# Optimization experiments

Measured on AMD Instinct MI355X. Metric: run time of the kernel, lower is better.

The kernel has to match this reference:

```python
import jax, jax.numpy as jnp
import numpy as np

MASK_VALUE = -1000000.0  # matches torch source's value=-1000000.0


def setup_inputs() -> dict:
    key = jax.random.key(0)
    kq, kk, kv, kl = jax.random.split(key, 4)
    B, S, D = 64, 1024, 64
    q = jax.random.normal(kq, (B, S, D), dtype=jnp.float32)
    k = jax.random.normal(kk, (B, S, D), dtype=jnp.float32)
    v = jax.random.normal(kv, (B, S, D), dtype=jnp.float32)
    valid_lens = jax.random.randint(kl, (B,), 0, S, dtype=jnp.int32)
    return {"q": q, "k": k, "v": v, "valid_lens": valid_lens}


def reference(q, k, v, valid_lens):
    # scores: [B, Sq, Sk]
    d = q.shape[-1]
    scores = jnp.einsum("bqd,bkd->bqk", q, k) / jnp.sqrt(jnp.float32(d))
    # 1-D valid_lens broadcast over the query dim (torch repeat_interleave branch)
    Sk = k.shape[1]
    mask = jnp.arange(Sk, dtype=jnp.int32)[None, None, :] < valid_lens[:, None, None]
    scores = jnp.where(mask, scores, MASK_VALUE)
    attn = jax.nn.softmax(scores, axis=-1)
    # dropout p=0.0 -> identity (eval-mode reference)
    return jnp.einsum("bqk,bkd->bqd", attn, v)
```

## Files before the change

kernel.cpp:

```cpp
#include <hip/hip_runtime.h>
#include <math.h>


#define BATCH 64
#define SEQ   1024
#define DIM   64
#define BQ    64
#define BC    64
#define NKT   (SEQ / BC)
#define HALFT 8
#define LSTR  72
#define QSCALE 0.18033688011112442f
#define MASKED -1.0e6f

#define WS_LM_SZ   (2048 * 64 * 8)
#define WS_O_OFF   WS_LM_SZ
#define WS_O_SZ    (2048 * 4096 * 4)
#define WS_NEEDED  ((size_t)WS_O_OFF + (size_t)WS_O_SZ)

typedef __attribute__((ext_vector_type(8))) short bf16x8;
typedef __attribute__((ext_vector_type(4))) float f32x4;

__device__ __forceinline__ uint pack2_trunc(float lo, float hi) {
    return __builtin_amdgcn_perm(__float_as_uint(hi), __float_as_uint(lo), 0x07060302);
}
__device__ __forceinline__ ushort f2bf_rne(float x) {
    uint u = __float_as_uint(x);
    return (ushort)((u + 0x7fffu + ((u >> 16) & 1u)) >> 16);
}

__global__ __launch_bounds__(256, 4) void attn_mfma_splitk(
    const float* __restrict__ q, const float* __restrict__ k,
    const float* __restrict__ v, const int* __restrict__ valid_lens,
    float* __restrict__ out,
    float2* __restrict__ lmbuf, float* __restrict__ opart)
{
    __shared__ ushort KPs[BC * LSTR];
    __shared__ ushort Vt[DIM * LSTR];

    const int t    = threadIdx.x;
    const int wave = t >> 6;
    const int wl   = t & 63;
    const int QD   = wl >> 4;
    const int li   = wl & 15;
    const int g    = blockIdx.x;
    const int grp  = g >> 6;
    const int b    = ((g & 63) + grp) & 63;
    const int half = grp & 1;
    const int qt   = grp >> 1;
    const int q0   = qt * BQ;
    const int pid  = (qt << 6) | b;
    const int item = pid * 2 + half;
    const int vl   = valid_lens[b];

    const size_t boff = (size_t)b * SEQ * DIM;

    const int it_full  = (vl == 0) ? NKT : ((vl + BC - 1) >> 6);
    const int it_begin = half * HALFT;
    const int it_end   = min(it_full, it_begin + HALFT);

    if (it_begin >= it_end) return;

    const bool direct = (half == 0) && (it_full <= HALFT);

    bf16x8 qb[2];
    {
        const float* qrow = q + boff + (size_t)(q0 + wave * 16 + li) * DIM + QD * 8;
        #pragma unroll
        for (int kc = 0; kc < 2; kc++) {
            float4 a = *(const float4*)(qrow + kc * 32);
            float4 c = *(const float4*)(qrow + kc * 32 + 4);
            union { bf16x8 v; ushort u[8]; } tmp;
            tmp.u[0] = f2bf_rne(a.x * QSCALE);
            tmp.u[1] = f2bf_rne(a.y * QSCALE);
            tmp.u[2] = f2bf_rne(a.z * QSCALE);
            tmp.u[3] = f2bf_rne(a.w * QSCALE);
            tmp.u[4] = f2bf_rne(c.x * QSCALE);
            tmp.u[5] = f2bf_rne(c.y * QSCALE);
            tmp.u[6] = f2bf_rne(c.z * QSCALE);
            tmp.u[7] = f2bf_rne(c.w * QSCALE);
            qb[kc] = tmp.v;
        }
    }

    float4 kf[4];
    float  vf[2][8];

    auto load_tile = [&](int it) {
        const float4* kg = (const float4*)(k + boff + (size_t)it * BC * DIM);
        #pragma unroll
        for (int i = 0; i < 4; i++) kf[i] = kg[t + 256 * i];
        const float* vgf = v + boff + (size_t)it * BC * DIM;
        #pragma unroll
        for (int i = 0; i < 2; i++) {
            int slot = t + 256 * i;
            int d = slot & 63, ko = slot >> 6;
            #pragma unroll
            for (int j = 0; j < 8; j++)
                vf[i][j] = vgf[(size_t)(ko * 8 + j) * DIM + d];
        }
    };

    auto stage = [&]() {
        #pragma unroll
        for (int i = 0; i < 4; i++) {
            int idx = t + 256 * i;
            int row = idx >> 4, c4 = idx & 15;
            uint2 w;
            w.x = pack2_trunc(kf[i].x, kf[i].y);
            w.y = pack2_trunc(kf[i].z, kf[i].w);
            *(uint2*)&KPs[row * LSTR + c4 * 4] = w;
        }
        #pragma unroll
        for (int i = 0; i < 2; i++) {
            int slot = t + 256 * i;
            int d = slot & 63, ko = slot >> 6;
            uint4 w;
            w.x = pack2_trunc(vf[i][0], vf[i][1]);
            w.y = pack2_trunc(vf[i][2], vf[i][3]);
            w.z = pack2_trunc(vf[i][4], vf[i][5]);
            w.w = pack2_trunc(vf[i][6], vf[i][7]);
            *(uint4*)&Vt[d * LSTR + ko * 8] = w;
        }
    };

    float m_run = -INFINITY, l_run = 0.f;
    f32x4 acc[4];
    #pragma unroll
    for (int dt = 0; dt < 4; dt++) acc[dt] = (f32x4){0.f, 0.f, 0.f, 0.f};

    load_tile(it_begin);

    for (int it = it_begin; it < it_end; it++) {
        __syncthreads();
        stage();
        if (it + 1 < it_end) load_tile(it + 1);
        __syncthreads();

        f32x4 sc[4];
        #pragma unroll
        for (int kt = 0; kt < 4; kt++) {
            bf16x8 ka0 = *(const bf16x8*)&KPs[(kt * 16 + li) * LSTR + QD * 8];
            bf16x8 ka1 = *(const bf16x8*)&KPs[(kt * 16 + li) * LSTR + 32 + QD * 8];
            f32x4 c = (f32x4){0.f, 0.f, 0.f, 0.f};
            c = __builtin_amdgcn_mfma_f32_16x16x32_bf16(ka0, qb[0], c, 0, 0, 0);
            c = __builtin_amdgcn_mfma_f32_16x16x32_bf16(ka1, qb[1], c, 0, 0, 0);
            sc[kt] = c;
        }

        __syncthreads();

        const int kbase = it * BC;
        if (kbase + BC > vl) {
            #pragma unroll
            for (int kt = 0; kt < 4; kt++)
                #pragma unroll
                for (int r = 0; r < 4; r++) {
                    int key = kbase + kt * 16 + QD * 4 + r;
                    if (key >= vl) sc[kt][r] = MASKED;
                }
        }

        float mt = -INFINITY;
        #pragma unroll
        for (int kt = 0; kt < 4; kt++)
            #pragma unroll
            for (int r = 0; r < 4; r++) mt = fmaxf(mt, sc[kt][r]);
        mt = fmaxf(mt, __shfl_xor(mt, 16, 64));
        mt = fmaxf(mt, __shfl_xor(mt, 32, 64));
        float mn = fmaxf(m_run, mt);
        float alpha = exp2f(m_run - mn);
        m_run = mn;

        float ls = 0.f;
        #pragma unroll
        for (int kt = 0; kt < 4; kt++) {
            float p0 = exp2f(sc[kt][0] - mn);
            float p1 = exp2f(sc[kt][1] - mn);
            float p2 = exp2f(sc[kt][2] - mn);
            float p3 = exp2f(sc[kt][3] - mn);
            ls += (p0 + p1) + (p2 + p3);
            uint2 w;
            w.x = pack2_trunc(p0, p1);
            w.y = pack2_trunc(p2, p3);
            *(uint2*)&KPs[(wave * 16 + li) * LSTR + kt * 16 + QD * 4] = w;
        }
        ls += __shfl_xor(ls, 16, 64);
        ls += __shfl_xor(ls, 32, 64);
        l_run = l_run * alpha + ls;

        float a0 = __shfl(alpha, QD * 4 + 0, 64);
        float a1 = __shfl(alpha, QD * 4 + 1, 64);
        float a2 = __shfl(alpha, QD * 4 + 2, 64);
        float a3 = __shfl(alpha, QD * 4 + 3, 64);
        #pragma unroll
        for (int dt = 0; dt < 4; dt++) {
            acc[dt][0] *= a0; acc[dt][1] *= a1;
            acc[dt][2] *= a2; acc[dt][3] *= a3;
        }

        bf16x8 pa0 = *(const bf16x8*)&KPs[(wave * 16 + li) * LSTR + QD * 8];
        bf16x8 pa1 = *(const bf16x8*)&KPs[(wave * 16 + li) * LSTR + 32 + QD * 8];
        #pragma unroll
        for (int dt = 0; dt < 4; dt++) {
            bf16x8 vb0 = *(const bf16x8*)&Vt[(dt * 16 + li) * LSTR + QD * 8];
            bf16x8 vb1 = *(const bf16x8*)&Vt[(dt * 16 + li) * LSTR + 32 + QD * 8];
            acc[dt] = __builtin_amdgcn_mfma_f32_16x16x32_bf16(pa0, vb0, acc[dt], 0, 0, 0);
            acc[dt] = __builtin_amdgcn_mfma_f32_16x16x32_bf16(pa1, vb1, acc[dt], 0, 0, 0);
        }
    }

    if (direct) {
        float invl = 1.0f / l_run;
        float i0 = __shfl(invl, QD * 4 + 0, 64);
        float i1 = __shfl(invl, QD * 4 + 1, 64);
        float i2 = __shfl(invl, QD * 4 + 2, 64);
        float i3 = __shfl(invl, QD * 4 + 3, 64);
        float* ob = out + boff + (size_t)q0 * DIM;
        const int rbase = wave * 16 + QD * 4;
        #pragma unroll
        for (int dt = 0; dt < 4; dt++) {
            int col = dt * 16 + li;
            ob[(size_t)(rbase + 0) * DIM + col] = acc[dt][0] * i0;
            ob[(size_t)(rbase + 1) * DIM + col] = acc[dt][1] * i1;
            ob[(size_t)(rbase + 2) * DIM + col] = acc[dt][2] * i2;
            ob[(size_t)(rbase + 3) * DIM + col] = acc[dt][3] * i3;
        }
    } else {
        if (QD == 0)
            lmbuf[(size_t)item * 64 + wave * 16 + li] = make_float2(m_run, l_run);
        float* ob = opart + (size_t)item * (BQ * DIM);
        const int rbase = wave * 16 + QD * 4;
        #pragma unroll
        for (int dt = 0; dt < 4; dt++) {
            int col = dt * 16 + li;
            ob[(size_t)(rbase + 0) * DIM + col] = acc[dt][0];
            ob[(size_t)(rbase + 1) * DIM + col] = acc[dt][1];
            ob[(size_t)(rbase + 2) * DIM + col] = acc[dt][2];
            ob[(size_t)(rbase + 3) * DIM + col] = acc[dt][3];
        }
    }
}

__global__ __launch_bounds__(256) void attn_combine(
    const int* __restrict__ valid_lens,
    const float2* __restrict__ lmbuf, const float* __restrict__ opart,
    float* __restrict__ out)
{
    const int pid = blockIdx.x;
    const int b   = pid & 63;
    const int qt  = pid >> 6;
    const int vl  = valid_lens[b];
    const int it_full = (vl == 0) ? NKT : ((vl + BC - 1) >> 6);
    if (it_full <= HALFT) return;

    const int t  = threadIdx.x;
    const int qr = t >> 2;
    const int c4 = t & 3;
    const int i1 = pid * 2;

    float2 ml1 = lmbuf[(size_t)i1 * 64 + qr];
    float2 ml2 = lmbuf[(size_t)(i1 + 1) * 64 + qr];
    float M  = fmaxf(ml1.x, ml2.x);
    float w1 = exp2f(ml1.x - M);
    float w2 = exp2f(ml2.x - M);
    float inv = 1.f / (ml1.y * w1 + ml2.y * w2);
    w1 *= inv; w2 *= inv;

    const float4* o1 = (const float4*)(opart + (size_t)i1 * (BQ * DIM));
    const float4* o2 = (const float4*)(opart + (size_t)(i1 + 1) * (BQ * DIM));
    float4* ob = (float4*)(out + ((size_t)b * SEQ + (size_t)qt * BQ) * DIM);
    #pragma unroll
    for (int j = 0; j < 4; j++) {
        int idx = qr * 16 + j * 4 + c4;
        float4 a  = o1[idx];
        float4 bb = o2[idx];
        float4 r;
        r.x = a.x * w1 + bb.x * w2;
        r.y = a.y * w1 + bb.y * w2;
        r.z = a.z * w1 + bb.z * w2;
        r.w = a.w * w1 + bb.w * w2;
        ob[idx] = r;
    }
}

__global__ __launch_bounds__(256, 4) void attn_mfma_flash2(
    const float* __restrict__ q, const float* __restrict__ k,
    const float* __restrict__ v, const int* __restrict__ valid_lens,
    float* __restrict__ out)
{
    __shared__ ushort Ks[BC * LSTR];
    __shared__ ushort Vt[DIM * LSTR];
    __shared__ ushort Ps[BQ * LSTR];

    const int t    = threadIdx.x;
    const int wave = t >> 6;
    const int wl   = t & 63;
    const int QD   = wl >> 4;
    const int li   = wl & 15;
    const int g    = blockIdx.x;
    const int grp  = g >> 6;
    const int b    = ((g & 63) + grp) & 63;
    const int q0   = grp * BQ;
    const int vl   = valid_lens[b];

    const size_t boff = (size_t)b * SEQ * DIM;

    bf16x8 qb[2];
    {
        const float* qrow = q + boff + (size_t)(q0 + wave * 16 + li) * DIM + QD * 8;
        #pragma unroll
        for (int kc = 0; kc < 2; kc++) {
            float4 a = *(const float4*)(qrow + kc * 32);
            float4 c = *(const float4*)(qrow + kc * 32 + 4);
            union { bf16x8 v; ushort u[8]; } tmp;
            tmp.u[0] = f2bf_rne(a.x * QSCALE);
            tmp.u[1] = f2bf_rne(a.y * QSCALE);
            tmp.u[2] = f2bf_rne(a.z * QSCALE);
            tmp.u[3] = f2bf_rne(a.w * QSCALE);
            tmp.u[4] = f2bf_rne(c.x * QSCALE);
            tmp.u[5] = f2bf_rne(c.y * QSCALE);
            tmp.u[6] = f2bf_rne(c.z * QSCALE);
            tmp.u[7] = f2bf_rne(c.w * QSCALE);
            qb[kc] = tmp.v;
        }
    }

    const int it_max = (vl == 0) ? NKT : ((vl + BC - 1) >> 6);

    float4 kf[4];
    float  vf[2][8];

    auto load_tile = [&](int it) {
        const float4* kg = (const float4*)(k + boff + (size_t)it * BC * DIM);
        #pragma unroll
        for (int i = 0; i < 4; i++) kf[i] = kg[t + 256 * i];
        const float* vgf = v + boff + (size_t)it * BC * DIM;
        #pragma unroll
        for (int i = 0; i < 2; i++) {
            int slot = t + 256 * i;
            int d = slot & 63, ko = slot >> 6;
            #pragma unroll
            for (int j = 0; j < 8; j++)
                vf[i][j] = vgf[(size_t)(ko * 8 + j) * DIM + d];
        }
    };

    auto stage = [&]() {
        #pragma unroll
        for (int i = 0; i < 4; i++) {
            int idx = t + 256 * i;
            int row = idx >> 4, c4 = idx & 15;
            uint2 w;
            w.x = pack2_trunc(kf[i].x, kf[i].y);
            w.y = pack2_trunc(kf[i].z, kf[i].w);
            *(uint2*)&Ks[row * LSTR + c4 * 4] = w;
        }
        #pragma unroll
        for (int i = 0; i < 2; i++) {
            int slot = t + 256 * i;
            int d = slot & 63, ko = slot >> 6;
            uint4 w;
            w.x = pack2_trunc(vf[i][0], vf[i][1]);
            w.y = pack2_trunc(vf[i][2], vf[i][3]);
            w.z = pack2_trunc(vf[i][4], vf[i][5]);
            w.w = pack2_trunc(vf[i][6], vf[i][7]);
            *(uint4*)&Vt[d * LSTR + ko * 8] = w;
        }
    };

    float m_run = -INFINITY, l_run = 0.f;
    f32x4 acc[4];
    #pragma unroll
    for (int dt = 0; dt < 4; dt++) acc[dt] = (f32x4){0.f, 0.f, 0.f, 0.f};

    load_tile(0);

    for (int it = 0; it < it_max; it++) {
        __syncthreads();
        stage();
        if (it + 1 < it_max) load_tile(it + 1);
        __syncthreads();

        f32x4 sc[4];
        #pragma unroll
        for (int kt = 0; kt < 4; kt++) {
            bf16x8 ka0 = *(const bf16x8*)&Ks[(kt * 16 + li) * LSTR + QD * 8];
            bf16x8 ka1 = *(const bf16x8*)&Ks[(kt * 16 + li) * LSTR + 32 + QD * 8];
            f32x4 c = (f32x4){0.f, 0.f, 0.f, 0.f};
            c = __builtin_amdgcn_mfma_f32_16x16x32_bf16(ka0, qb[0], c, 0, 0, 0);
            c = __builtin_amdgcn_mfma_f32_16x16x32_bf16(ka1, qb[1], c, 0, 0, 0);
            sc[kt] = c;
        }

        const int kbase = it * BC;
        if (kbase + BC > vl) {
            #pragma unroll
            for (int kt = 0; kt < 4; kt++)
                #pragma unroll
                for (int r = 0; r < 4; r++) {
                    int key = kbase + kt * 16 + QD * 4 + r;
                    if (key >= vl) sc[kt][r] = MASKED;
                }
        }

        float mt = -INFINITY;
        #pragma unroll
        for (int kt = 0; kt < 4; kt++)
            #pragma unroll
            for (int r = 0; r < 4; r++) mt = fmaxf(mt, sc[kt][r]);
        mt = fmaxf(mt, __shfl_xor(mt, 16, 64));
        mt = fmaxf(mt, __shfl_xor(mt, 32, 64));
        float mn = fmaxf(m_run, mt);
        float alpha = exp2f(m_run - mn);
        m_run = mn;

        float ls = 0.f;
        #pragma unroll
        for (int kt = 0; kt < 4; kt++) {
            float p0 = exp2f(sc[kt][0] - mn);
            float p1 = exp2f(sc[kt][1] - mn);
            float p2 = exp2f(sc[kt][2] - mn);
            float p3 = exp2f(sc[kt][3] - mn);
            ls += (p0 + p1) + (p2 + p3);
            uint2 w;
            w.x = pack2_trunc(p0, p1);
            w.y = pack2_trunc(p2, p3);
            *(uint2*)&Ps[(wave * 16 + li) * LSTR + kt * 16 + QD * 4] = w;
        }
        ls += __shfl_xor(ls, 16, 64);
        ls += __shfl_xor(ls, 32, 64);
        l_run = l_run * alpha + ls;

        float a0 = __shfl(alpha, QD * 4 + 0, 64);
        float a1 = __shfl(alpha, QD * 4 + 1, 64);
        float a2 = __shfl(alpha, QD * 4 + 2, 64);
        float a3 = __shfl(alpha, QD * 4 + 3, 64);
        #pragma unroll
        for (int dt = 0; dt < 4; dt++) {
            acc[dt][0] *= a0; acc[dt][1] *= a1;
            acc[dt][2] *= a2; acc[dt][3] *= a3;
        }

        bf16x8 pa0 = *(const bf16x8*)&Ps[(wave * 16 + li) * LSTR + QD * 8];
        bf16x8 pa1 = *(const bf16x8*)&Ps[(wave * 16 + li) * LSTR + 32 + QD * 8];
        #pragma unroll
        for (int dt = 0; dt < 4; dt++) {
            bf16x8 vb0 = *(const bf16x8*)&Vt[(dt * 16 + li) * LSTR + QD * 8];
            bf16x8 vb1 = *(const bf16x8*)&Vt[(dt * 16 + li) * LSTR + 32 + QD * 8];
            acc[dt] = __builtin_amdgcn_mfma_f32_16x16x32_bf16(pa0, vb0, acc[dt], 0, 0, 0);
            acc[dt] = __builtin_amdgcn_mfma_f32_16x16x32_bf16(pa1, vb1, acc[dt], 0, 0, 0);
        }
    }

    float invl = 1.0f / l_run;
    float i0 = __shfl(invl, QD * 4 + 0, 64);
    float i1 = __shfl(invl, QD * 4 + 1, 64);
    float i2 = __shfl(invl, QD * 4 + 2, 64);
    float i3 = __shfl(invl, QD * 4 + 3, 64);
    float* ob = out + boff + (size_t)q0 * DIM;
    const int rbase = wave * 16 + QD * 4;
    #pragma unroll
    for (int dt = 0; dt < 4; dt++) {
        int col = dt * 16 + li;
        ob[(size_t)(rbase + 0) * DIM + col] = acc[dt][0] * i0;
        ob[(size_t)(rbase + 1) * DIM + col] = acc[dt][1] * i1;
        ob[(size_t)(rbase + 2) * DIM + col] = acc[dt][2] * i2;
        ob[(size_t)(rbase + 3) * DIM + col] = acc[dt][3] * i3;
    }
}

extern "C" void kernel_launch(void* const* d_in, const int* in_sizes, int n_in,
                              void* d_out, int out_size, void* d_ws, size_t ws_size,
                              hipStream_t stream) {
    const float* q = (const float*)d_in[0];
    const float* k = (const float*)d_in[1];
    const float* v = (const float*)d_in[2];
    const int* valid_lens = (const int*)d_in[3];
    float* out = (float*)d_out;

    if (d_ws != nullptr && ws_size >= WS_NEEDED) {
        float2* lmbuf = (float2*)d_ws;
        float*  opart = (float*)((char*)d_ws + WS_O_OFF);
        attn_mfma_splitk<<<dim3(BATCH * (SEQ / BQ) * 2), dim3(256), 0, stream>>>(
            q, k, v, valid_lens, out, lmbuf, opart);
        attn_combine<<<dim3(BATCH * (SEQ / BQ)), dim3(256), 0, stream>>>(
            valid_lens, lmbuf, opart, out);
    } else {
        dim3 grid(BATCH * (SEQ / BQ));
        attn_mfma_flash2<<<grid, dim3(256), 0, stream>>>(q, k, v, valid_lens, out);
    }
}
```

Before: 136.6 us.

## Keep softmax probabilities in registers and add lazy max rescaling

Builds the P operand for the PV MFMA directly in registers. To make the register fragment layout match, the V key ordering is permuted at load time, which removes the LDS write/read round trip for P and one block barrier per tile. Max rescaling becomes lazy: the running max and accumulators are updated only when some lane's tile max exceeds the running max by more than a threshold. The row-sum reduction across lanes is deferred to the end. Barriers become raw s_barrier calls with explicit lgkmcnt waits. The lazy max lets exp2 arguments grow up to 2^8, which trades a little precision headroom for skipping rescale work.

```diff
diff --git a/kernel.cpp b/kernel.cpp
--- a/kernel.cpp
+++ b/kernel.cpp
@@ -12,6 +12,7 @@
 #define LSTR  72
 #define QSCALE 0.18033688011112442f
 #define MASKED -1.0e6f
+#define THR    8.0f
 
 #define WS_LM_SZ   (2048 * 64 * 8)
 #define WS_O_OFF   WS_LM_SZ
@@ -29,13 +30,13 @@
     return (ushort)((u + 0x7fffu + ((u >> 16) & 1u)) >> 16);
 }
 
-__global__ __launch_bounds__(256, 4) void attn_mfma_splitk(
+__global__ __launch_bounds__(256, 4) void attn_splitk_lean(
     const float* __restrict__ q, const float* __restrict__ k,
     const float* __restrict__ v, const int* __restrict__ valid_lens,
     float* __restrict__ out,
     float2* __restrict__ lmbuf, float* __restrict__ opart)
 {
-    __shared__ ushort KPs[BC * LSTR];
+    __shared__ ushort Ks[BC * LSTR];
     __shared__ ushort Vt[DIM * LSTR];
 
     const int t    = threadIdx.x;
@@ -58,7 +59,6 @@
     const int it_full  = (vl == 0) ? NKT : ((vl + BC - 1) >> 6);
     const int it_begin = half * HALFT;
     const int it_end   = min(it_full, it_begin + HALFT);
-
     if (it_begin >= it_end) return;
 
     const bool direct = (half == 0) && (it_full <= HALFT);
@@ -95,9 +95,12 @@
         for (int i = 0; i < 2; i++) {
             int slot = t + 256 * i;
             int d = slot & 63, ko = slot >> 6;
-            #pragma unroll
-            for (int j = 0; j < 8; j++)
-                vf[i][j] = vgf[(size_t)(ko * 8 + j) * DIM + d];
+            int kb = (ko >> 2) * 16 + (ko & 3) * 4;
+            #pragma unroll
+            for (int j = 0; j < 8; j++) {
+                int kk = kb + ((j >> 2) << 5) + (j & 3);
+                vf[i][j] = vgf[(size_t)kk * DIM + d];
+            }
         }
     };
 
@@ -109,7 +112,7 @@
             uint2 w;
             w.x = pack2_trunc(kf[i].x, kf[i].y);
             w.y = pack2_trunc(kf[i].z, kf[i].w);
-            *(uint2*)&KPs[row * LSTR + c4 * 4] = w;
+            *(uint2*)&Ks[row * LSTR + c4 * 4] = w;
         }
         #pragma unroll
         for (int i = 0; i < 2; i++) {
@@ -124,7 +127,8 @@
         }
     };
 
-    float m_run = -INFINITY, l_run = 0.f;
+    float m_run = -INFINITY;
+    float l_run = 0.f;
     f32x4 acc[4];
     #pragma unroll
     for (int dt = 0; dt < 4; dt++) acc[dt] = (f32x4){0.f, 0.f, 0.f, 0.f};
@@ -132,23 +136,28 @@
     load_tile(it_begin);
 
     for (int it = it_begin; it < it_end; it++) {
-        __syncthreads();
+        __builtin_amdgcn_sched_barrier(0);
+        __builtin_amdgcn_s_barrier();
+        __builtin_amdgcn_sched_barrier(0);
+
         stage();
         if (it + 1 < it_end) load_tile(it + 1);
-        __syncthreads();
+
+        __builtin_amdgcn_sched_barrier(0);
+        asm volatile("s_waitcnt lgkmcnt(0)" ::: "memory");
+        __builtin_amdgcn_s_barrier();
+        __builtin_amdgcn_sched_barrier(0);
 
         f32x4 sc[4];
         #pragma unroll
         for (int kt = 0; kt < 4; kt++) {
-            bf16x8 ka0 = *(const bf16x8*)&KPs[(kt * 16 + li) * LSTR + QD * 8];
-            bf16x8 ka1 = *(const bf16x8*)&KPs[(kt * 16 + li) * LSTR + 32 + QD * 8];
+            bf16x8 ka0 = *(const bf16x8*)&Ks[(kt * 16 + li) * LSTR + QD * 8];
+            bf16x8 ka1 = *(const bf16x8*)&Ks[(kt * 16 + li) * LSTR + 32 + QD * 8];
             f32x4 c = (f32x4){0.f, 0.f, 0.f, 0.f};
             c = __builtin_amdgcn_mfma_f32_16x16x32_bf16(ka0, qb[0], c, 0, 0, 0);
             c = __builtin_amdgcn_mfma_f32_16x16x32_bf16(ka1, qb[1], c, 0, 0, 0);
             sc[kt] = c;
         }
-
-        __syncthreads();
 
         const int kbase = it * BC;
         if (kbase + BC > vl) {
@@ -166,49 +175,58 @@
         for (int kt = 0; kt < 4; kt++)
             #pragma unroll
             for (int r = 0; r < 4; r++) mt = fmaxf(mt, sc[kt][r]);
-        mt = fmaxf(mt, __shfl_xor(mt, 16, 64));
-        mt = fmaxf(mt, __shfl_xor(mt, 32, 64));
-        float mn = fmaxf(m_run, mt);
-        float alpha = exp2f(m_run - mn);
-        m_run = mn;
-
-        float ls = 0.f;
-        #pragma unroll
-        for (int kt = 0; kt < 4; kt++) {
-            float p0 = exp2f(sc[kt][0] - mn);
-            float p1 = exp2f(sc[kt][1] - mn);
-            float p2 = exp2f(sc[kt][2] - mn);
-            float p3 = exp2f(sc[kt][3] - mn);
-            ls += (p0 + p1) + (p2 + p3);
-            uint2 w;
-            w.x = pack2_trunc(p0, p1);
-            w.y = pack2_trunc(p2, p3);
-            *(uint2*)&KPs[(wave * 16 + li) * LSTR + kt * 16 + QD * 4] = w;
-        }
-        ls += __shfl_xor(ls, 16, 64);
-        ls += __shfl_xor(ls, 32, 64);
-        l_run = l_run * alpha + ls;
-
-        float a0 = __shfl(alpha, QD * 4 + 0, 64);
-        float a1 = __shfl(alpha, QD * 4 + 1, 64);
-        float a2 = __shfl(alpha, QD * 4 + 2, 64);
-        float a3 = __shfl(alpha, QD * 4 + 3, 64);
-        #pragma unroll
-        for (int dt = 0; dt < 4; dt++) {
-            acc[dt][0] *= a0; acc[dt][1] *= a1;
-            acc[dt][2] *= a2; acc[dt][3] *= a3;
-        }
-
-        bf16x8 pa0 = *(const bf16x8*)&KPs[(wave * 16 + li) * LSTR + QD * 8];
-        bf16x8 pa1 = *(const bf16x8*)&KPs[(wave * 16 + li) * LSTR + 32 + QD * 8];
+
+        if (!__all(mt - m_run <= THR)) {
+            mt = fmaxf(mt, __shfl_xor(mt, 16, 64));
+            mt = fmaxf(mt, __shfl_xor(mt, 32, 64));
+            float mn = fmaxf(m_run, mt);
+            float alpha = exp2f(m_run - mn);
+            m_run = mn;
+            l_run *= alpha;
+            float a0 = __shfl(alpha, QD * 4 + 0, 64);
+            float a1 = __shfl(alpha, QD * 4 + 1, 64);
+            float a2 = __shfl(alpha, QD * 4 + 2, 64);
+            float a3 = __shfl(alpha, QD * 4 + 3, 64);
+            #pragma unroll
+            for (int dt = 0; dt < 4; dt++) {
+                acc[dt][0] *= a0; acc[dt][1] *= a1;
+                acc[dt][2] *= a2; acc[dt][3] *= a3;
+            }
+        }
+
+        union { bf16x8 v; uint u[4]; } pa0u, pa1u;
+        {
+            float p00 = exp2f(sc[0][0] - m_run), p01 = exp2f(sc[0][1] - m_run);
+            float p02 = exp2f(sc[0][2] - m_run), p03 = exp2f(sc[0][3] - m_run);
+            float p10 = exp2f(sc[1][0] - m_run), p11 = exp2f(sc[1][1] - m_run);
+            float p12 = exp2f(sc[1][2] - m_run), p13 = exp2f(sc[1][3] - m_run);
+            float p20 = exp2f(sc[2][0] - m_run), p21 = exp2f(sc[2][1] - m_run);
+            float p22 = exp2f(sc[2][2] - m_run), p23 = exp2f(sc[2][3] - m_run);
+            float p30 = exp2f(sc[3][0] - m_run), p31 = exp2f(sc[3][1] - m_run);
+            float p32 = exp2f(sc[3][2] - m_run), p33 = exp2f(sc[3][3] - m_run);
+            l_run += ((p00 + p01) + (p02 + p03)) + ((p10 + p11) + (p12 + p13))
+                   + ((p20 + p21) + (p22 + p23)) + ((p30 + p31) + (p32 + p33));
+            pa0u.u[0] = pack2_trunc(p00, p01);
+            pa0u.u[1] = pack2_trunc(p02, p03);
+            pa0u.u[2] = pack2_trunc(p20, p21);
+            pa0u.u[3] = pack2_trunc(p22, p23);
+            pa1u.u[0] = pack2_trunc(p10, p11);
+            pa1u.u[1] = pack2_trunc(p12, p13);
+            pa1u.u[2] = pack2_trunc(p30, p31);
+            pa1u.u[3] = pack2_trunc(p32, p33);
+        }
+
         #pragma unroll
         for (int dt = 0; dt < 4; dt++) {
             bf16x8 vb0 = *(const bf16x8*)&Vt[(dt * 16 + li) * LSTR + QD * 8];
             bf16x8 vb1 = *(const bf16x8*)&Vt[(dt * 16 + li) * LSTR + 32 + QD * 8];
-            acc[dt] = __builtin_amdgcn_mfma_f32_16x16x32_bf16(pa0, vb0, acc[dt], 0, 0, 0);
-            acc[dt] = __builtin_amdgcn_mfma_f32_16x16x32_bf16(pa1, vb1, acc[dt], 0, 0, 0);
-        }
-    }
+            acc[dt] = __builtin_amdgcn_mfma_f32_16x16x32_bf16(pa0u.v, vb0, acc[dt], 0, 0, 0);
+            acc[dt] = __builtin_amdgcn_mfma_f32_16x16x32_bf16(pa1u.v, vb1, acc[dt], 0, 0, 0);
+        }
+    }
+
+    l_run += __shfl_xor(l_run, 16, 64);
+    l_run += __shfl_xor(l_run, 32, 64);
 
     if (direct) {
         float invl = 1.0f / l_run;
@@ -284,24 +302,21 @@
     }
 }
 
-__global__ __launch_bounds__(256, 4) void attn_mfma_flash2(
+__global__ __launch_bounds__(256, 4) void attn_mfma_flash4(
     const float* __restrict__ q, const float* __restrict__ k,
     const float* __restrict__ v, const int* __restrict__ valid_lens,
     float* __restrict__ out)
 {
     __shared__ ushort Ks[BC * LSTR];
     __shared__ ushort Vt[DIM * LSTR];
-    __shared__ ushort Ps[BQ * LSTR];
 
     const int t    = threadIdx.x;
     const int wave = t >> 6;
     const int wl   = t & 63;
     const int QD   = wl >> 4;
     const int li   = wl & 15;
-    const int g    = blockIdx.x;
-    const int grp  = g >> 6;
-    const int b    = ((g & 63) + grp) & 63;
-    const int q0   = grp * BQ;
+    const int b    = blockIdx.x & 63;
+    const int q0   = (blockIdx.x >> 6) * BQ;
     const int vl   = valid_lens[b];
 
     const size_t boff = (size_t)b * SEQ * DIM;
@@ -340,9 +355,12 @@
         for (int i = 0; i < 2; i++) {
             int slot = t + 256 * i;
             int d = slot & 63, ko = slot >> 6;
-            #pragma unroll
-            for (int j = 0; j < 8; j++)
-                vf[i][j] = vgf[(size_t)(ko * 8 + j) * DIM + d];
+            int kb = (ko >> 2) * 16 + (ko & 3) * 4;
+            #pragma unroll
+            for (int j = 0; j < 8; j++) {
+                int kk = kb + ((j >> 2) << 5) + (j & 3);
+                vf[i][j] = vgf[(size_t)kk * DIM + d];
+            }
         }
     };
 
@@ -377,10 +395,17 @@
     load_tile(0);
 
     for (int it = 0; it < it_max; it++) {
-        __syncthreads();
+        __builtin_amdgcn_sched_barrier(0);
+        __builtin_amdgcn_s_barrier();
+        __builtin_amdgcn_sched_barrier(0);
+
         stage();
         if (it + 1 < it_max) load_tile(it + 1);
-        __syncthreads();
+
+        __builtin_amdgcn_sched_barrier(0);
+        asm volatile("s_waitcnt lgkmcnt(0)" ::: "memory");
+        __builtin_amdgcn_s_barrier();
+        __builtin_amdgcn_sched_barrier(0);
 
         f32x4 sc[4];
         #pragma unroll
@@ -409,50 +434,58 @@
         for (int kt = 0; kt < 4; kt++)
             #pragma unroll
             for (int r = 0; r < 4; r++) mt = fmaxf(mt, sc[kt][r]);
-        mt = fmaxf(mt, __shfl_xor(mt, 16, 64));
-        mt = fmaxf(mt, __shfl_xor(mt, 32, 64));
-        float mn = fmaxf(m_run, mt);
-        float alpha = exp2f(m_run - mn);
-        m_run = mn;
-
-        float ls = 0.f;
-        #pragma unroll
-        for (int kt = 0; kt < 4; kt++) {
-            float p0 = exp2f(sc[kt][0] - mn);
-            float p1 = exp2f(sc[kt][1] - mn);
-            float p2 = exp2f(sc[kt][2] - mn);
-            float p3 = exp2f(sc[kt][3] - mn);
-            ls += (p0 + p1) + (p2 + p3);
-            uint2 w;
-            w.x = pack2_trunc(p0, p1);
-            w.y = pack2_trunc(p2, p3);
-            *(uint2*)&Ps[(wave * 16 + li) * LSTR + kt * 16 + QD * 4] = w;
-        }
-        ls += __shfl_xor(ls, 16, 64);
-        ls += __shfl_xor(ls, 32, 64);
-        l_run = l_run * alpha + ls;
-
-        float a0 = __shfl(alpha, QD * 4 + 0, 64);
-        float a1 = __shfl(alpha, QD * 4 + 1, 64);
-        float a2 = __shfl(alpha, QD * 4 + 2, 64);
-        float a3 = __shfl(alpha, QD * 4 + 3, 64);
-        #pragma unroll
-        for (int dt = 0; dt < 4; dt++) {
-            acc[dt][0] *= a0; acc[dt][1] *= a1;
-            acc[dt][2] *= a2; acc[dt][3] *= a3;
-        }
-
-        bf16x8 pa0 = *(const bf16x8*)&Ps[(wave * 16 + li) * LSTR + QD * 8];
-        bf16x8 pa1 = *(const bf16x8*)&Ps[(wave * 16 + li) * LSTR + 32 + QD * 8];
+
+        if (!__all(mt - m_run <= THR)) {
+            mt = fmaxf(mt, __shfl_xor(mt, 16, 64));
+            mt = fmaxf(mt, __shfl_xor(mt, 32, 64));
+            float mn = fmaxf(m_run, mt);
+            float alpha = exp2f(m_run - mn);
+            m_run = mn;
+            l_run *= alpha;
+            float a0 = __shfl(alpha, QD * 4 + 0, 64);
+            float a1 = __shfl(alpha, QD * 4 + 1, 64);
+            float a2 = __shfl(alpha, QD * 4 + 2, 64);
+            float a3 = __shfl(alpha, QD * 4 + 3, 64);
+            #pragma unroll
+            for (int dt = 0; dt < 4; dt++) {
+                acc[dt][0] *= a0; acc[dt][1] *= a1;
+                acc[dt][2] *= a2; acc[dt][3] *= a3;
+            }
+        }
+
+        union { bf16x8 v; uint u[4]; } pa0u, pa1u;
+        {
+            float p00 = exp2f(sc[0][0] - m_run), p01 = exp2f(sc[0][1] - m_run);
+            float p02 = exp2f(sc[0][2] - m_run), p03 = exp2f(sc[0][3] - m_run);
+            float p10 = exp2f(sc[1][0] - m_run), p11 = exp2f(sc[1][1] - m_run);
+            float p12 = exp2f(sc[1][2] - m_run), p13 = exp2f(sc[1][3] - m_run);
+            float p20 = exp2f(sc[2][0] - m_run), p21 = exp2f(sc[2][1] - m_run);
+            float p22 = exp2f(sc[2][2] - m_run), p23 = exp2f(sc[2][3] - m_run);
+            float p30 = exp2f(sc[3][0] - m_run), p31 = exp2f(sc[3][1] - m_run);
+            float p32 = exp2f(sc[3][2] - m_run), p33 = exp2f(sc[3][3] - m_run);
+            l_run += ((p00 + p01) + (p02 + p03)) + ((p10 + p11) + (p12 + p13))
+                   + ((p20 + p21) + (p22 + p23)) + ((p30 + p31) + (p32 + p33));
+            pa0u.u[0] = pack2_trunc(p00, p01);
+            pa0u.u[1] = pack2_trunc(p02, p03);
+            pa0u.u[2] = pack2_trunc(p20, p21);
+            pa0u.u[3] = pack2_trunc(p22, p23);
+            pa1u.u[0] = pack2_trunc(p10, p11);
+            pa1u.u[1] = pack2_trunc(p12, p13);
+            pa1u.u[2] = pack2_trunc(p30, p31);
+            pa1u.u[3] = pack2_trunc(p32, p33);
+        }
+
         #pragma unroll
         for (int dt = 0; dt < 4; dt++) {
             bf16x8 vb0 = *(const bf16x8*)&Vt[(dt * 16 + li) * LSTR + QD * 8];
             bf16x8 vb1 = *(const bf16x8*)&Vt[(dt * 16 + li) * LSTR + 32 + QD * 8];
-            acc[dt] = __builtin_amdgcn_mfma_f32_16x16x32_bf16(pa0, vb0, acc[dt], 0, 0, 0);
-            acc[dt] = __builtin_amdgcn_mfma_f32_16x16x32_bf16(pa1, vb1, acc[dt], 0, 0, 0);
-        }
-    }
-
+            acc[dt] = __builtin_amdgcn_mfma_f32_16x16x32_bf16(pa0u.v, vb0, acc[dt], 0, 0, 0);
+            acc[dt] = __builtin_amdgcn_mfma_f32_16x16x32_bf16(pa1u.v, vb1, acc[dt], 0, 0, 0);
+        }
+    }
+
+    l_run += __shfl_xor(l_run, 16, 64);
+    l_run += __shfl_xor(l_run, 32, 64);
     float invl = 1.0f / l_run;
     float i0 = __shfl(invl, QD * 4 + 0, 64);
     float i1 = __shfl(invl, QD * 4 + 1, 64);
@@ -482,12 +515,12 @@
     if (d_ws != nullptr && ws_size >= WS_NEEDED) {
         float2* lmbuf = (float2*)d_ws;
         float*  opart = (float*)((char*)d_ws + WS_O_OFF);
-        attn_mfma_splitk<<<dim3(BATCH * (SEQ / BQ) * 2), dim3(256), 0, stream>>>(
+        attn_splitk_lean<<<dim3(BATCH * (SEQ / BQ) * 2), dim3(256), 0, stream>>>(
             q, k, v, valid_lens, out, lmbuf, opart);
         attn_combine<<<dim3(BATCH * (SEQ / BQ)), dim3(256), 0, stream>>>(
             valid_lens, lmbuf, opart, out);
     } else {
-        dim3 grid(BATCH * (SEQ / BQ));
-        attn_mfma_flash2<<<grid, dim3(256), 0, stream>>>(q, k, v, valid_lens, out);
+        attn_mfma_flash4<<<dim3(BATCH * (SEQ / BQ)), dim3(256), 0, stream>>>(
+            q, k, v, valid_lens, out);
     }
 }
```

Result: no change. 134.7 us (-1.4%).
